# Kernel tuning notes

Measured on AMD Instinct MI355X. Metric: run time of the kernel, lower is better.

Reference implementation:

```python
import jax, jax.numpy as jnp
import numpy as np

L, N, K, S, V, H = 12, 2048, 8, 4, 50000, 256


def setup_inputs() -> dict:
    key = jax.random.key(0)
    ks = jax.random.split(key, 20)
    tokens1 = jax.random.randint(ks[0], (L, N, S), 0, V, dtype=jnp.int32)
    tokens2 = jax.random.randint(ks[1], (L, N, S), 0, V, dtype=jnp.int32)
    # child indices into previous level's h (0 = zero-init row, -1 = no child)
    idx1 = jax.random.randint(ks[2], (L, N, K), -1, N + 1, dtype=jnp.int32).at[0].set(-1)
    idx2 = jax.random.randint(ks[3], (L, N, K), -1, N + 1, dtype=jnp.int32).at[0].set(-1)
    sc = 0.02
    E = jax.random.normal(ks[4], (V, H), jnp.float32)  # torch.randn init
    lin_W = jax.random.normal(ks[5], (H * S, H), jnp.float32) * sc
    lin_b = jnp.zeros((H,), jnp.float32)
    Uf_W = jax.random.normal(ks[6], (H, H), jnp.float32) * sc
    Uf_b = jnp.zeros((H,), jnp.float32)
    Uiuo_W = jax.random.normal(ks[7], (H, 3 * H), jnp.float32) * sc
    Uiuo_b = jnp.zeros((3 * H,), jnp.float32)
    W_W = jax.random.normal(ks[8], (H, 4 * H), jnp.float32) * sc
    W_b = jnp.zeros((4 * H,), jnp.float32)
    dense_W = jax.random.normal(ks[9], (H, 512), jnp.float32) * sc
    dense_b = jnp.zeros((512,), jnp.float32)
    out_W = jax.random.normal(ks[10], (512, 2), jnp.float32) * sc
    out_b = jnp.zeros((2,), jnp.float32)
    return dict(tokens1=tokens1, idx1=idx1, tokens2=tokens2, idx2=idx2,
                E=E, lin_W=lin_W, lin_b=lin_b, Uf_W=Uf_W, Uf_b=Uf_b,
                Uiuo_W=Uiuo_W, Uiuo_b=Uiuo_b, W_W=W_W, W_b=W_b,
                dense_W=dense_W, dense_b=dense_b, out_W=out_W, out_b=out_b)


def _encode(tokens, idx, E, lin_W, lin_b, Uf_W, Uf_b, Uiuo_W, Uiuo_b, W_W, W_b):
    # TreeEmbeddingLayer: lookup label_size tokens per node, concat, linear
    emb = E[tokens].reshape(L, N, S * H)           # [L,N,S*H]
    x = emb @ lin_W + lin_b                        # [L,N,H]

    def step(carry, inp):
        h_prev, c_prev = carry                     # [N,H]
        xl, il = inp                               # [N,H], [N,K]
        zero = jnp.zeros((1, H), xl.dtype)
        hp = jnp.concatenate([zero, h_prev], 0)    # [N+1,H] (row 0 = init)
        cp = jnp.concatenate([zero, c_prev], 0)
        mask_bool = il != -1
        index = jnp.where(mask_bool, il, 0)
        h = hp[index]                              # [N,K,H] gather child states
        c = cp[index]
        m = mask_bool[..., None].astype(xl.dtype)  # [N,K,1]
        h_sum = jnp.sum(h * m, axis=1)             # [N,H]
        Wx = xl @ W_W + W_b                        # [N,4H]
        Wf, Wi, Wu, Wo = Wx[:, :H], Wx[:, H:2*H], Wx[:, 2*H:3*H], Wx[:, 3*H:]
        fk = jax.nn.sigmoid(Wf[:, None, :] + h @ Uf_W + Uf_b)  # [N,K,H]
        bf = jnp.sum(fk * c * m, axis=1)           # [N,H]
        iuo = h_sum @ Uiuo_W + Uiuo_b              # [N,3H]
        i = jax.nn.sigmoid(iuo[:, :H] + Wi)
        u = jnp.tanh(iuo[:, H:2*H] + Wu)
        o = jax.nn.sigmoid(iuo[:, 2*H:] + Wo)
        nc = i * u + bf
        nh = o * jnp.tanh(nc)
        return (nh, nc), nh

    init = (jnp.zeros((N, H), x.dtype), jnp.zeros((N, H), x.dtype))
    (_, _), hs = jax.lax.scan(step, init, (x, idx))
    # 1 layer with skip connection; hx = last (root) level
    return hs[-1] + x[-1]                          # [N,H]


def reference(tokens1, idx1, tokens2, idx2, E, lin_W, lin_b, Uf_W, Uf_b,
              Uiuo_W, Uiuo_b, W_W, W_b, dense_W, dense_b, out_W, out_b):
    h1 = _encode(tokens1, idx1, E, lin_W, lin_b, Uf_W, Uf_b, Uiuo_W, Uiuo_b, W_W, W_b)
    h2 = _encode(tokens2, idx2, E, lin_W, lin_b, Uf_W, Uf_b, Uiuo_W, Uiuo_b, W_W, W_b)
    abs_dist = jnp.abs(h1 - h2)                    # [N,H]
    x = jnp.tanh(abs_dist @ dense_W + dense_b)     # dropout = identity (eval)
    logits = x @ out_W + out_b                     # [N,2]
    return jax.nn.softmax(logits, axis=-1)
```

## Files before the change

### kernel.cpp

```cpp
#include <hip/hip_runtime.h>

#define LL 12
#define NN 2048
#define KK 8
#define SS 4
#define HH 256
#define LN (LL*NN)
#define VV 50000
#define ZROW 4096
#define SROW 2048

typedef __bf16 bf16_t;
typedef __bf16 bf16x8 __attribute__((ext_vector_type(8)));
typedef __bf16 bf16x4v __attribute__((ext_vector_type(4)));
typedef float f32x4 __attribute__((ext_vector_type(4)));

__device__ __forceinline__ float sigmoidf_(float x) { return 1.f / (1.f + expf(-x)); }

__global__ __launch_bounds__(256) void k_cvtE(const float* __restrict__ src,
                                              bf16_t* __restrict__ dst, int n4)
{
    int i = blockIdx.x * 256 + threadIdx.x;
    const int stride = gridDim.x * 256;
    for (; i < n4; i += stride) {
        const float4 v = ((const float4*)src)[i];
        bf16x4v o;
        o[0] = (bf16_t)v.x; o[1] = (bf16_t)v.y; o[2] = (bf16_t)v.z; o[3] = (bf16_t)v.w;
        ((bf16x4v*)dst)[i] = o;
    }
}

__global__ __launch_bounds__(256) void k_cvtW(
    const float* __restrict__ linW, const float* __restrict__ WW,
    const float* __restrict__ UfW, const float* __restrict__ UiW,
    bf16_t* __restrict__ linWt, bf16_t* __restrict__ WWt,
    bf16_t* __restrict__ UfWt, bf16_t* __restrict__ UiWt)
{
    int i = blockIdx.x * 256 + threadIdx.x;
    if (i < 262144) {
        const int rr = i >> 8, cc = i & 255;
        linWt[(size_t)cc * 1024 + rr] = (bf16_t)linW[i];
        return;
    }
    i -= 262144;
    if (i < 262144) {
        const int rr = i >> 10, cc = i & 1023;
        WWt[(size_t)cc * 256 + rr] = (bf16_t)WW[i];
        return;
    }
    i -= 262144;
    if (i < 65536) {
        const int rr = i >> 8, cc = i & 255;
        UfWt[(size_t)cc * 256 + rr] = (bf16_t)UfW[i];
        return;
    }
    i -= 65536;
    if (i < 196608) {
        const int rr = i / 768, cc = i - rr * 768;
        UiWt[(size_t)cc * 256 + rr] = (bf16_t)UiW[i];
    }
}

__global__ __launch_bounds__(256) void k_zero(float* __restrict__ SA, float* __restrict__ SB)
{
    const int t = threadIdx.x;
    float* a = SA + (size_t)ZROW * 512;
    float* b = SB + (size_t)ZROW * 512;
    a[t] = 0.f; a[t + 256] = 0.f;
    b[t] = 0.f; b[t + 256] = 0.f;
}

__global__ __launch_bounds__(256) void k_embed(
    const int* __restrict__ tok1, const int* __restrict__ tok2,
    const bf16_t* __restrict__ Ebf, const bf16_t* __restrict__ linWt,
    const float* __restrict__ linb, bf16_t* __restrict__ xout)
{
    __shared__ int toff[64][SS];
    const int t = threadIdx.x;
    const int m0 = blockIdx.x * 64;
    {
        const int lr = t >> 2, s = t & 3;
        const int m = m0 + lr;
        const int e = (m >= LN) ? 1 : 0;
        const int rrow = m - e * LN;
        const int* tok = e ? tok2 : tok1;
        toff[lr][s] = tok[(size_t)rrow * SS + s] * HH;
    }
    __syncthreads();
    const int lane = t & 63, w = t >> 6;
    const int wm = w >> 1, wn = w & 1;
    const int r = lane & 15, kg = lane >> 4;
    const int lr0 = wm * 32 + r, lr1 = lr0 + 16;
    const bf16_t* bp[8];
    #pragma unroll
    for (int j = 0; j < 8; ++j)
        bp[j] = linWt + (size_t)(wn * 128 + j * 16 + r) * 1024 + kg * 8;

    const f32x4 zero = {0.f, 0.f, 0.f, 0.f};
    f32x4 acc[2][8];
    #pragma unroll
    for (int mi = 0; mi < 2; ++mi)
        #pragma unroll
        for (int j = 0; j < 8; ++j) acc[mi][j] = zero;

    for (int k0 = 0; k0 < 1024; k0 += 32) {
        const int s = k0 >> 8, off = (k0 & 255) + kg * 8;
        const bf16x8 a0 = *(const bf16x8*)(Ebf + (size_t)toff[lr0][s] + off);
        const bf16x8 a1 = *(const bf16x8*)(Ebf + (size_t)toff[lr1][s] + off);
        #pragma unroll
        for (int j = 0; j < 8; ++j) {
            const bf16x8 b = *(const bf16x8*)bp[j];
            acc[0][j] = __builtin_amdgcn_mfma_f32_16x16x32_bf16(a0, b, acc[0][j], 0, 0, 0);
            acc[1][j] = __builtin_amdgcn_mfma_f32_16x16x32_bf16(a1, b, acc[1][j], 0, 0, 0);
            bp[j] += 32;
        }
    }
    const int crow = m0 + wm * 32 + kg * 4;
    #pragma unroll
    for (int j = 0; j < 8; ++j) {
        const int ccol = wn * 128 + j * 16 + r;
        const float bv = linb[ccol];
        #pragma unroll
        for (int mi = 0; mi < 2; ++mi)
            #pragma unroll
            for (int jj = 0; jj < 4; ++jj)
                xout[(size_t)(crow + mi * 16 + jj) * HH + ccol] =
                    (bf16_t)(acc[mi][j][jj] + bv);
    }
}

__global__ __launch_bounds__(512) void k_step(
    const bf16_t* __restrict__ xbf,
    const int* __restrict__ idx1, const int* __restrict__ idx2, const int l,
    const bf16_t* __restrict__ UfWt, const float* __restrict__ Ufb,
    const bf16_t* __restrict__ UiWt, const float* __restrict__ Uib,
    const bf16_t* __restrict__ WWt, const float* __restrict__ Wb,
    const char* __restrict__ Sprev, char* __restrict__ Snext)
{
    __shared__ __align__(16) bf16_t WxL[16 * 1024];
    __shared__ __align__(16) bf16_t iuoL[16 * 768];
    __shared__ __align__(16) bf16_t hsumL[16 * 256];
    __shared__ __align__(16) float  bfaL[16 * 256];

    const int t = threadIdx.x;
    const int bid = blockIdx.x;
    const int x  = bid & 7;
    const int e  = x >> 2;
    const int n0 = ((bid >> 3) * 4 + (x & 3)) * 16;
    const int g0 = e * NN + n0;
    const int lane = t & 63, w = t >> 6;
    const int r = lane & 15, kg = lane >> 4;
    const f32x4 zero = {0.f, 0.f, 0.f, 0.f};

    const bf16_t* xrow = xbf + ((size_t)e * LN + (size_t)l * NN + n0 + r) * HH + kg * 8;
    bf16x8 aWx[8];
    #pragma unroll
    for (int k = 0; k < 8; ++k) aWx[k] = *(const bf16x8*)(xrow + k * 32);

    {
        const bf16_t* bw[8];
        #pragma unroll
        for (int j = 0; j < 8; ++j)
            bw[j] = WWt + (size_t)((8 * w + j) * 16 + r) * HH + kg * 8;
        f32x4 acc[8];
        #pragma unroll
        for (int j = 0; j < 8; ++j) acc[j] = zero;
        #pragma unroll
        for (int k = 0; k < 8; ++k) {
            #pragma unroll
            for (int j = 0; j < 8; ++j) {
                const bf16x8 b = *(const bf16x8*)bw[j];
                acc[j] = __builtin_amdgcn_mfma_f32_16x16x32_bf16(aWx[k], b, acc[j], 0, 0, 0);
                bw[j] += 32;
            }
        }
        #pragma unroll
        for (int j = 0; j < 8; ++j) {
            const int col = (8 * w + j) * 16 + r;
            const float bv = Wb[col];
            #pragma unroll
            for (int jj = 0; jj < 4; ++jj)
                WxL[(size_t)(kg * 4 + jj) * 1024 + col] = (bf16_t)(acc[j][jj] + bv);
        }
    }
    __syncthreads();

    {
        const int rr = t >> 5, sl = t & 31;
        const int colb = sl * 8;
        const int* idxp = (e ? idx2 : idx1) + ((size_t)l * NN + n0 + rr) * KK;
        const int4 i0 = *(const int4*)idxp;
        const int4 i1 = *(const int4*)(idxp + 4);
        int ch[KK];
        ch[0] = i0.x; ch[1] = i0.y; ch[2] = i0.z; ch[3] = i0.w;
        ch[4] = i1.x; ch[5] = i1.y; ch[6] = i1.z; ch[7] = i1.w;
        #pragma unroll
        for (int k = 0; k < KK; ++k)
            ch[k] = (ch[k] >= 1) ? (e * NN + ch[k] - 1) : ZROW;

        float wf[8];
        {
            const bf16x8 wv = *(const bf16x8*)(WxL + (size_t)rr * 1024 + colb);
            #pragma unroll
            for (int j = 0; j < 8; ++j) wf[j] = (float)wv[j];
        }
        float hs[8] = {0.f, 0.f, 0.f, 0.f, 0.f, 0.f, 0.f, 0.f};
        float ba[8] = {0.f, 0.f, 0.f, 0.f, 0.f, 0.f, 0.f, 0.f};
        #pragma unroll
        for (int k = 0; k < KK; ++k) {
            const char* row = Sprev + (size_t)ch[k] * SROW;
            const float4 c0 = *(const float4*)(row + sl * 32);
            const float4 c1 = *(const float4*)(row + sl * 32 + 16);
            const bf16x8 hv = *(const bf16x8*)(row + 1024 + sl * 16);
            const bf16x8 fv = *(const bf16x8*)(row + 1536 + sl * 16);
            const float cc[8] = {c0.x, c0.y, c0.z, c0.w, c1.x, c1.y, c1.z, c1.w};
            #pragma unroll
            for (int j = 0; j < 8; ++j) {
                hs[j] += (float)hv[j];
                const float fk = sigmoidf_(wf[j] + (float)fv[j]);
                ba[j] = fmaf(fk, cc[j], ba[j]);
            }
        }
        bf16x8 o;
        #pragma unroll
        for (int j = 0; j < 8; ++j) o[j] = (bf16_t)hs[j];
        const int ss = (sl + 4 * (rr & 7)) & 31;
        *(bf16x8*)(hsumL + (size_t)rr * 256 + ss * 8) = o;
        f32x4 b0 = {ba[0], ba[1], ba[2], ba[3]};
        f32x4 b1 = {ba[4], ba[5], ba[6], ba[7]};
        *(f32x4*)(bfaL + (size_t)rr * 256 + colb) = b0;
        *(f32x4*)(bfaL + (size_t)rr * 256 + colb + 4) = b1;
    }
    __syncthreads();

    {
        const bf16_t* bu[6];
        #pragma unroll
        for (int j = 0; j < 6; ++j)
            bu[j] = UiWt + (size_t)((6 * w + j) * 16 + r) * HH + kg * 8;
        f32x4 acc[6];
        #pragma unroll
        for (int j = 0; j < 6; ++j) acc[j] = zero;
        for (int k0 = 0; k0 < HH; k0 += 32) {
            const int ss = (((k0 >> 3) + kg) + 4 * (r & 7)) & 31;
            const bf16x8 a = *(const bf16x8*)(hsumL + (size_t)r * 256 + ss * 8);
            #pragma unroll
            for (int j = 0; j < 6; ++j) {
                const bf16x8 b = *(const bf16x8*)bu[j];
                acc[j] = __builtin_amdgcn_mfma_f32_16x16x32_bf16(a, b, acc[j], 0, 0, 0);
                bu[j] += 32;
            }
        }
        #pragma unroll
        for (int j = 0; j < 6; ++j) {
            const int col = (6 * w + j) * 16 + r;
            const float bv = Uib[col];
            #pragma unroll
            for (int jj = 0; jj < 4; ++jj)
                iuoL[(size_t)(kg * 4 + jj) * 768 + col] = (bf16_t)(acc[j][jj] + bv);
        }
    }
    __syncthreads();

    {
        const int col = t & 255, rb2 = t >> 8;
        for (int i = 0; i < 8; ++i) {
            const int rr = i * 2 + rb2;
            const int g = g0 + rr;
            const float Wi = (float)WxL[(size_t)rr * 1024 + 256 + col];
            const float Wu = (float)WxL[(size_t)rr * 1024 + 512 + col];
            const float Wo = (float)WxL[(size_t)rr * 1024 + 768 + col];
            const float ba = bfaL[(size_t)rr * 256 + col];
            const float ig = sigmoidf_((float)iuoL[(size_t)rr * 768 + col] + Wi);
            const float ug = tanhf((float)iuoL[(size_t)rr * 768 + 256 + col] + Wu);
            const float og = sigmoidf_((float)iuoL[(size_t)rr * 768 + 512 + col] + Wo);
            const float nc = fmaf(ig, ug, ba);
            const float nh = og * tanhf(nc);
            char* rowN = Snext + (size_t)g * SROW;
            ((float*)rowN)[col] = nc;
            const bf16_t nhb = (bf16_t)nh;
            ((bf16_t*)(rowN + 1024))[col] = nhb;
            const int ss2 = ((col >> 3) + 4 * (rr & 7)) & 31;
            hsumL[(size_t)rr * 256 + ss2 * 8 + (col & 7)] = nhb;
        }
    }

    if (l < LL - 1) {
        __syncthreads();
        const int ct0 = 2 * w;
        const bf16_t* bq0 = UfWt + (size_t)(ct0 * 16 + r) * HH + kg * 8;
        const bf16_t* bq1 = bq0 + (size_t)16 * HH;
        f32x4 ac0 = zero, ac1 = zero;
        for (int k0 = 0; k0 < HH; k0 += 32) {
            const int ss = (((k0 >> 3) + kg) + 4 * (r & 7)) & 31;
            const bf16x8 a = *(const bf16x8*)(hsumL + (size_t)r * 256 + ss * 8);
            const bf16x8 b0 = *(const bf16x8*)bq0;
            const bf16x8 b1 = *(const bf16x8*)bq1;
            ac0 = __builtin_amdgcn_mfma_f32_16x16x32_bf16(a, b0, ac0, 0, 0, 0);
            ac1 = __builtin_amdgcn_mfma_f32_16x16x32_bf16(a, b1, ac1, 0, 0, 0);
            bq0 += 32; bq1 += 32;
        }
        const int c0 = ct0 * 16 + r, c1 = c0 + 16;
        const float bv0 = Ufb[c0], bv1 = Ufb[c1];
        #pragma unroll
        for (int jj = 0; jj < 4; ++jj) {
            bf16_t* fr = (bf16_t*)(Snext + (size_t)(g0 + kg * 4 + jj) * SROW + 1536);
            fr[c0] = (bf16_t)(ac0[jj] + bv0);
            fr[c1] = (bf16_t)(ac1[jj] + bv1);
        }
    }
}

__global__ __launch_bounds__(256) void k_final(
    const char* __restrict__ Sfin, const bf16_t* __restrict__ xbf,
    const float* __restrict__ dW, const float* __restrict__ db,
    const float* __restrict__ oW, const float* __restrict__ ob,
    float* __restrict__ out)
{
    __shared__ __align__(16) float ad[8][HH];
    __shared__ __align__(16) float xx[8][512];
    const int t = threadIdx.x;
    const int n0 = blockIdx.x * 8;
    const size_t xoff1 = (size_t)(LL - 1) * NN * HH;
    const size_t xoff2 = (size_t)LN * HH + xoff1;
    #pragma unroll
    for (int rr = 0; rr < 8; ++rr) {
        const int n = n0 + rr;
        const float h1 = (float)((const bf16_t*)(Sfin + (size_t)n * SROW + 1024))[t]
                       + (float)xbf[xoff1 + (size_t)n * HH + t];
        const float h2 = (float)((const bf16_t*)(Sfin + (size_t)(NN + n) * SROW + 1024))[t]
                       + (float)xbf[xoff2 + (size_t)n * HH + t];
        ad[rr][t] = fabsf(h1 - h2);
    }
    __syncthreads();
    float a0[8], a1[8];
    #pragma unroll
    for (int rr = 0; rr < 8; ++rr) { a0[rr] = 0.f; a1[rr] = 0.f; }
    for (int k = 0; k < HH; k += 4) {
        #pragma unroll
        for (int kk = 0; kk < 4; ++kk) {
            const float b0 = dW[(size_t)(k + kk) * 512 + t];
            const float b1 = dW[(size_t)(k + kk) * 512 + 256 + t];
            #pragma unroll
            for (int rr = 0; rr < 8; ++rr) {
                const float av = ad[rr][k + kk];
                a0[rr] = fmaf(av, b0, a0[rr]);
                a1[rr] = fmaf(av, b1, a1[rr]);
            }
        }
    }
    const float db0 = db[t], db1 = db[256 + t];
    #pragma unroll
    for (int rr = 0; rr < 8; ++rr) {
        xx[rr][t] = tanhf(a0[rr] + db0);
        xx[rr][256 + t] = tanhf(a1[rr] + db1);
    }
    __syncthreads();
    const int w = t >> 6, lane = t & 63;
    for (int rr = w; rr < 8; rr += 4) {
        float p0 = 0.f, p1 = 0.f;
        for (int k = lane; k < 512; k += 64) {
            const float xv = xx[rr][k];
            p0 = fmaf(xv, oW[2 * k + 0], p0);
            p1 = fmaf(xv, oW[2 * k + 1], p1);
        }
        #pragma unroll
        for (int off = 32; off > 0; off >>= 1) {
            p0 += __shfl_down(p0, off);
            p1 += __shfl_down(p1, off);
        }
        if (lane == 0) {
            const float l0 = p0 + ob[0], l1 = p1 + ob[1];
            const float mx = fmaxf(l0, l1);
            const float e0 = expf(l0 - mx), e1 = expf(l1 - mx);
            const float inv = 1.f / (e0 + e1);
            out[(size_t)(n0 + rr) * 2 + 0] = e0 * inv;
            out[(size_t)(n0 + rr) * 2 + 1] = e1 * inv;
        }
    }
}

extern "C" void kernel_launch(void* const* d_in, const int* in_sizes, int n_in,
                              void* d_out, int out_size, void* d_ws, size_t ws_size,
                              hipStream_t stream) {
    (void)in_sizes; (void)n_in; (void)out_size; (void)ws_size;
    const int*   tok1 = (const int*)d_in[0];
    const int*   idx1 = (const int*)d_in[1];
    const int*   tok2 = (const int*)d_in[2];
    const int*   idx2 = (const int*)d_in[3];
    const float* E    = (const float*)d_in[4];
    const float* linW = (const float*)d_in[5];
    const float* linb = (const float*)d_in[6];
    const float* UfW  = (const float*)d_in[7];
    const float* Ufb  = (const float*)d_in[8];
    const float* UiW  = (const float*)d_in[9];
    const float* Uib  = (const float*)d_in[10];
    const float* WW   = (const float*)d_in[11];
    const float* Wb   = (const float*)d_in[12];
    const float* dW   = (const float*)d_in[13];
    const float* db   = (const float*)d_in[14];
    const float* oW   = (const float*)d_in[15];
    const float* ob   = (const float*)d_in[16];
    float* out = (float*)d_out;

    bf16_t* xbf = (bf16_t*)d_ws;
    char*   uni = (char*)(xbf + (size_t)12582912);
    bf16_t* Ebf = (bf16_t*)uni;
    char*   SA  = uni;
    char*   SB  = uni + 8390656;
    bf16_t* linWt = (bf16_t*)(uni + 25600000);
    bf16_t* WWt   = linWt + (size_t)262144;
    bf16_t* UfWt  = WWt   + (size_t)262144;
    bf16_t* UiWt  = UfWt  + (size_t)65536;

    k_cvtE<<<2048, 256, 0, stream>>>(E, Ebf, VV * HH / 4);
    k_cvtW<<<3072, 256, 0, stream>>>(linW, WW, UfW, UiW, linWt, WWt, UfWt, UiWt);

    k_embed<<<768, 256, 0, stream>>>(tok1, tok2, Ebf, linWt, linb, xbf);

    k_zero<<<1, 256, 0, stream>>>((float*)SA, (float*)SB);

    char *Sp = SA, *Sn = SB;
    for (int l = 0; l < LL; ++l) {
        k_step<<<256, 512, 0, stream>>>(xbf, idx1, idx2, l,
                                        UfWt, Ufb, UiWt, Uib, WWt, Wb, Sp, Sn);
        char* ts = Sp; Sp = Sn; Sn = ts;
    }

    k_final<<<NN / 8, 256, 0, stream>>>(Sp, xbf, dW, db, oW, ob, out);
}
```

Before: 719.2 us.

## Prefetch child gathers early and overlap them with MFMA phases in step kernel

Moves the child-index loads and the h gathers to the start of the step kernel so their latency overlaps the Wx MFMA. The c and f gathers are issued before the iuo MFMA, and the forget-gate reduction is kept in registers, which drops the bfaL shared buffer and one barrier. The final gate phase is vectorised to 8 columns per thread, and launch bounds now request 2 blocks per CU. The cost is much higher register pressure from holding the prefetched rows, which may cause spills or lower occupancy.

```diff
diff --git a/kernel.cpp b/kernel.cpp
--- a/kernel.cpp
+++ b/kernel.cpp
@@ -129,7 +129,7 @@
     }
 }
 
-__global__ __launch_bounds__(512) void k_step(
+__global__ __launch_bounds__(512, 2) void k_step(
     const bf16_t* __restrict__ xbf,
     const int* __restrict__ idx1, const int* __restrict__ idx2, const int l,
     const bf16_t* __restrict__ UfWt, const float* __restrict__ Ufb,
@@ -140,7 +140,6 @@
     __shared__ __align__(16) bf16_t WxL[16 * 1024];
     __shared__ __align__(16) bf16_t iuoL[16 * 768];
     __shared__ __align__(16) bf16_t hsumL[16 * 256];
-    __shared__ __align__(16) float  bfaL[16 * 256];
 
     const int t = threadIdx.x;
     const int bid = blockIdx.x;
@@ -152,6 +151,26 @@
     const int r = lane & 15, kg = lane >> 4;
     const f32x4 zero = {0.f, 0.f, 0.f, 0.f};
 
+    const int rr = t >> 5, sl = t & 31;
+    const int ss = (sl + 4 * (rr & 7)) & 31;
+
+    int ch[KK];
+    {
+        const int* idxp = (e ? idx2 : idx1) + ((size_t)l * NN + n0 + rr) * KK;
+        const int4 i0 = *(const int4*)idxp;
+        const int4 i1 = *(const int4*)(idxp + 4);
+        ch[0] = i0.x; ch[1] = i0.y; ch[2] = i0.z; ch[3] = i0.w;
+        ch[4] = i1.x; ch[5] = i1.y; ch[6] = i1.z; ch[7] = i1.w;
+        #pragma unroll
+        for (int k = 0; k < KK; ++k)
+            ch[k] = (ch[k] >= 1) ? (e * NN + ch[k] - 1) : ZROW;
+    }
+
+    bf16x8 hv[KK];
+    #pragma unroll
+    for (int k = 0; k < KK; ++k)
+        hv[k] = *(const bf16x8*)(Sprev + (size_t)ch[k] * SROW + 1024 + sl * 16);
+
     const bf16_t* xrow = xbf + ((size_t)e * LN + (size_t)l * NN + n0 + r) * HH + kg * 8;
     bf16x8 aWx[8];
     #pragma unroll
@@ -183,55 +202,30 @@
                 WxL[(size_t)(kg * 4 + jj) * 1024 + col] = (bf16_t)(acc[j][jj] + bv);
         }
     }
+
+    {
+        float hs[8] = {0.f, 0.f, 0.f, 0.f, 0.f, 0.f, 0.f, 0.f};
+        #pragma unroll
+        for (int k = 0; k < KK; ++k) {
+            #pragma unroll
+            for (int j = 0; j < 8; ++j) hs[j] += (float)hv[k][j];
+        }
+        bf16x8 o;
+        #pragma unroll
+        for (int j = 0; j < 8; ++j) o[j] = (bf16_t)hs[j];
+        *(bf16x8*)(hsumL + rr * 256 + ss * 8) = o;
+    }
     __syncthreads();
 
-    {
-        const int rr = t >> 5, sl = t & 31;
-        const int colb = sl * 8;
-        const int* idxp = (e ? idx2 : idx1) + ((size_t)l * NN + n0 + rr) * KK;
-        const int4 i0 = *(const int4*)idxp;
-        const int4 i1 = *(const int4*)(idxp + 4);
-        int ch[KK];
-        ch[0] = i0.x; ch[1] = i0.y; ch[2] = i0.z; ch[3] = i0.w;
-        ch[4] = i1.x; ch[5] = i1.y; ch[6] = i1.z; ch[7] = i1.w;
-        #pragma unroll
-        for (int k = 0; k < KK; ++k)
-            ch[k] = (ch[k] >= 1) ? (e * NN + ch[k] - 1) : ZROW;
-
-        float wf[8];
-        {
-            const bf16x8 wv = *(const bf16x8*)(WxL + (size_t)rr * 1024 + colb);
-            #pragma unroll
-            for (int j = 0; j < 8; ++j) wf[j] = (float)wv[j];
-        }
-        float hs[8] = {0.f, 0.f, 0.f, 0.f, 0.f, 0.f, 0.f, 0.f};
-        float ba[8] = {0.f, 0.f, 0.f, 0.f, 0.f, 0.f, 0.f, 0.f};
-        #pragma unroll
-        for (int k = 0; k < KK; ++k) {
-            const char* row = Sprev + (size_t)ch[k] * SROW;
-            const float4 c0 = *(const float4*)(row + sl * 32);
-            const float4 c1 = *(const float4*)(row + sl * 32 + 16);
-            const bf16x8 hv = *(const bf16x8*)(row + 1024 + sl * 16);
-            const bf16x8 fv = *(const bf16x8*)(row + 1536 + sl * 16);
-            const float cc[8] = {c0.x, c0.y, c0.z, c0.w, c1.x, c1.y, c1.z, c1.w};
-            #pragma unroll
-            for (int j = 0; j < 8; ++j) {
-                hs[j] += (float)hv[j];
-                const float fk = sigmoidf_(wf[j] + (float)fv[j]);
-                ba[j] = fmaf(fk, cc[j], ba[j]);
-            }
-        }
-        bf16x8 o;
-        #pragma unroll
-        for (int j = 0; j < 8; ++j) o[j] = (bf16_t)hs[j];
-        const int ss = (sl + 4 * (rr & 7)) & 31;
-        *(bf16x8*)(hsumL + (size_t)rr * 256 + ss * 8) = o;
-        f32x4 b0 = {ba[0], ba[1], ba[2], ba[3]};
-        f32x4 b1 = {ba[4], ba[5], ba[6], ba[7]};
-        *(f32x4*)(bfaL + (size_t)rr * 256 + colb) = b0;
-        *(f32x4*)(bfaL + (size_t)rr * 256 + colb + 4) = b1;
-    }
-    __syncthreads();
+    float4 cv0[KK], cv1[KK];
+    bf16x8 fv[KK];
+    #pragma unroll
+    for (int k = 0; k < KK; ++k) {
+        const char* row = Sprev + (size_t)ch[k] * SROW;
+        cv0[k] = *(const float4*)(row + sl * 32);
+        cv1[k] = *(const float4*)(row + sl * 32 + 16);
+        fv[k]  = *(const bf16x8*)(row + 1536 + sl * 16);
+    }
 
     {
         const bf16_t* bu[6];
@@ -242,8 +236,8 @@
         #pragma unroll
         for (int j = 0; j < 6; ++j) acc[j] = zero;
         for (int k0 = 0; k0 < HH; k0 += 32) {
-            const int ss = (((k0 >> 3) + kg) + 4 * (r & 7)) & 31;
-            const bf16x8 a = *(const bf16x8*)(hsumL + (size_t)r * 256 + ss * 8);
+            const int sa = (((k0 >> 3) + kg) + 4 * (r & 7)) & 31;
+            const bf16x8 a = *(const bf16x8*)(hsumL + r * 256 + sa * 8);
             #pragma unroll
             for (int j = 0; j < 6; ++j) {
                 const bf16x8 b = *(const bf16x8*)bu[j];
@@ -260,29 +254,50 @@
                 iuoL[(size_t)(kg * 4 + jj) * 768 + col] = (bf16_t)(acc[j][jj] + bv);
         }
     }
+
+    float ba[8] = {0.f, 0.f, 0.f, 0.f, 0.f, 0.f, 0.f, 0.f};
+    {
+        float wf[8];
+        const bf16x8 wv = *(const bf16x8*)(WxL + (size_t)rr * 1024 + sl * 8);
+        #pragma unroll
+        for (int j = 0; j < 8; ++j) wf[j] = (float)wv[j];
+        #pragma unroll
+        for (int k = 0; k < KK; ++k) {
+            const float cc[8] = {cv0[k].x, cv0[k].y, cv0[k].z, cv0[k].w,
+                                 cv1[k].x, cv1[k].y, cv1[k].z, cv1[k].w};
+            #pragma unroll
+            for (int j = 0; j < 8; ++j) {
+                const float fk = sigmoidf_(wf[j] + (float)fv[k][j]);
+                ba[j] = fmaf(fk, cc[j], ba[j]);
+            }
+        }
+    }
     __syncthreads();
 
     {
-        const int col = t & 255, rb2 = t >> 8;
-        for (int i = 0; i < 8; ++i) {
-            const int rr = i * 2 + rb2;
-            const int g = g0 + rr;
-            const float Wi = (float)WxL[(size_t)rr * 1024 + 256 + col];
-            const float Wu = (float)WxL[(size_t)rr * 1024 + 512 + col];
-            const float Wo = (float)WxL[(size_t)rr * 1024 + 768 + col];
-            const float ba = bfaL[(size_t)rr * 256 + col];
-            const float ig = sigmoidf_((float)iuoL[(size_t)rr * 768 + col] + Wi);
-            const float ug = tanhf((float)iuoL[(size_t)rr * 768 + 256 + col] + Wu);
-            const float og = sigmoidf_((float)iuoL[(size_t)rr * 768 + 512 + col] + Wo);
-            const float nc = fmaf(ig, ug, ba);
-            const float nh = og * tanhf(nc);
-            char* rowN = Snext + (size_t)g * SROW;
-            ((float*)rowN)[col] = nc;
-            const bf16_t nhb = (bf16_t)nh;
-            ((bf16_t*)(rowN + 1024))[col] = nhb;
-            const int ss2 = ((col >> 3) + 4 * (rr & 7)) & 31;
-            hsumL[(size_t)rr * 256 + ss2 * 8 + (col & 7)] = nhb;
-        }
+        const bf16x8 wiv = *(const bf16x8*)(WxL + (size_t)rr * 1024 + 256 + sl * 8);
+        const bf16x8 wuv = *(const bf16x8*)(WxL + (size_t)rr * 1024 + 512 + sl * 8);
+        const bf16x8 wov = *(const bf16x8*)(WxL + (size_t)rr * 1024 + 768 + sl * 8);
+        const bf16x8 iv  = *(const bf16x8*)(iuoL + (size_t)rr * 768 + sl * 8);
+        const bf16x8 uv  = *(const bf16x8*)(iuoL + (size_t)rr * 768 + 256 + sl * 8);
+        const bf16x8 ov  = *(const bf16x8*)(iuoL + (size_t)rr * 768 + 512 + sl * 8);
+        float nc[8];
+        bf16x8 nhb;
+        #pragma unroll
+        for (int j = 0; j < 8; ++j) {
+            const float ig = sigmoidf_((float)iv[j] + (float)wiv[j]);
+            const float ug = tanhf((float)uv[j] + (float)wuv[j]);
+            const float og = sigmoidf_((float)ov[j] + (float)wov[j]);
+            nc[j] = fmaf(ig, ug, ba[j]);
+            nhb[j] = (bf16_t)(og * tanhf(nc[j]));
+        }
+        char* rowN = Snext + (size_t)(g0 + rr) * SROW;
+        const f32x4 c0 = {nc[0], nc[1], nc[2], nc[3]};
+        const f32x4 c1 = {nc[4], nc[5], nc[6], nc[7]};
+        *(f32x4*)(rowN + sl * 32) = c0;
+        *(f32x4*)(rowN + sl * 32 + 16) = c1;
+        *(bf16x8*)(rowN + 1024 + sl * 16) = nhb;
+        *(bf16x8*)(hsumL + rr * 256 + ss * 8) = nhb;
     }
 
     if (l < LL - 1) {
@@ -292,8 +307,8 @@
         const bf16_t* bq1 = bq0 + (size_t)16 * HH;
         f32x4 ac0 = zero, ac1 = zero;
         for (int k0 = 0; k0 < HH; k0 += 32) {
-            const int ss = (((k0 >> 3) + kg) + 4 * (r & 7)) & 31;
-            const bf16x8 a = *(const bf16x8*)(hsumL + (size_t)r * 256 + ss * 8);
+            const int sa = (((k0 >> 3) + kg) + 4 * (r & 7)) & 31;
+            const bf16x8 a = *(const bf16x8*)(hsumL + r * 256 + sa * 8);
             const bf16x8 b0 = *(const bf16x8*)bq0;
             const bf16x8 b1 = *(const bf16x8*)bq1;
             ac0 = __builtin_amdgcn_mfma_f32_16x16x32_bf16(a, b0, ac0, 0, 0, 0);
```

Measured after the change: 707.0 us. About the same (-1.7%).
